# Kernel optimization log

Measured on AMD Instinct MI355X. Metric: run time of the kernel, lower is better.

The kernel has to match this reference:

```python
import jax, jax.numpy as jnp
import numpy as np

DELTA = 0.1  # fixed Gaussian temperature from __init__


def setup_inputs() -> dict:
    key = jax.random.key(0)
    k1, k2 = jax.random.split(key)
    B, T_TEXT, C = 16, 1024, 512
    T_FEAT = 4096  # static upper bound on sum(durations) per row (durations < 5 -> max 4*1024)
    x = jax.random.normal(k1, (B, T_TEXT, C), dtype=jnp.float32)
    durations = jax.random.randint(k2, (B, T_TEXT), 0, 5, dtype=jnp.int32)
    text_mask = jnp.ones((B, T_TEXT), dtype=bool)  # seqs_layout: valid text positions
    return {"x": x, "durations": durations, "text_mask": text_mask, "t_feat": T_FEAT}


def reference(x, durations, text_mask, t_feat):
    # x: (B, T_text, C); durations: (B, T_text) int; text_mask: (B, T_text) bool
    dtype = x.dtype
    d = durations.astype(dtype)
    out_lens = d.sum(axis=1)                                   # (B,)
    t = jnp.arange(t_feat, dtype=dtype)[None, :]               # (1, T_feat)
    y_mask = t < out_lens[:, None]                             # (B, T_feat) valid frames
    t = t * y_mask.astype(dtype)                               # zero out padded frames
    c = jnp.cumsum(d, axis=-1) - d * 0.5                       # (B, T_text) token centers
    # Gaussian energy over (frame, token) pairs: (B, T_feat, T_text)
    energy = -DELTA * (t[:, :, None] - c[:, None, :]) ** 2
    energy = jnp.where(text_mask[:, None, :], energy, -jnp.inf)
    p_attn = jax.nn.softmax(energy, axis=2)                    # softmax over T_text
    y = jnp.einsum("bft,btc->bfc", p_attn, x)                  # (B, T_feat, C)
    return y, out_lens.astype(jnp.int32)
```

## Files before the change

kernel.cpp:

```cpp
#include <hip/hip_runtime.h>
#include <stdint.h>


#define T_TEXT 1024
#define NEGK -0.14426950408889634f
#define WIN 12
#define WIN2F 169.0f

__global__ __launch_bounds__(1024) void scan_kernel(const int* __restrict__ dur,
                                                    const float* __restrict__ x,
                                                    float* __restrict__ c,
                                                    int* __restrict__ lens,
                                                    float* __restrict__ out_lens_f,
                                                    unsigned short* __restrict__ ft,
                                                    float* __restrict__ t0row,
                                                    int F) {
    const int b = blockIdx.x, tid = threadIdx.x;
    const int lane = tid & 63, wid = tid >> 6;
    const int d = dur[b * T_TEXT + tid];
    unsigned short* ftb = ft + (size_t)b * F;
    ((uint2*)ftb)[tid] = make_uint2(0x04000400u, 0x04000400u);

    __shared__ int wsum[16];
    __shared__ float clds[T_TEXT];
    __shared__ int sjhi0;
    if (tid == 0) sjhi0 = T_TEXT;

    int v = d;
#pragma unroll
    for (int off = 1; off < 64; off <<= 1) {
        int n = __shfl_up(v, off);
        if (lane >= off) v += n;
    }
    if (lane == 63) wsum[wid] = v;
    __syncthreads();
    if (tid < 16) {
        int s = wsum[tid];
#pragma unroll
        for (int off = 1; off < 16; off <<= 1) {
            int n = __shfl_up(s, off);
            if (tid >= off) s += n;
        }
        wsum[tid] = s;
    }
    __syncthreads();
    const int cum = v + (wid ? wsum[wid - 1] : 0);
    const float cv = (float)cum - 0.5f * (float)d;
    c[b * T_TEXT + tid] = cv;
    clds[tid] = cv;
    if (cum > WIN + 2 && cum - d <= WIN + 2) sjhi0 = tid;
    if (tid == T_TEXT - 1) { lens[b] = cum; out_lens_f[b] = (float)cum; }
    const int start = cum - d;
    for (int k = 0; k < d; ++k) ftb[start + k] = (unsigned short)tid;
    __syncthreads();

    const int jhi0 = sjhi0;
    if (tid < 512) {
        const float* xb = x + (size_t)b * T_TEXT * 512 + tid;
        float acc = 0.f, den = 0.f;
        for (int j = 0; j < jhi0; ++j) {
            const float cj = clds[j];
            const float w = exp2f(NEGK * cj * cj);
            acc += w * xb[(size_t)j * 512];
            den += w;
        }
        t0row[b * 512 + tid] = acc / den;
    }
}

__global__ __launch_bounds__(256, 4) void gauss_kernel(const float* __restrict__ x,
                                                       const float* __restrict__ c,
                                                       const int* __restrict__ lens,
                                                       const unsigned short* __restrict__ ft,
                                                       const float* __restrict__ t0row,
                                                       float* __restrict__ y,
                                                       int F) {
    const int C = 512;
    int bid = blockIdx.x;
    const int nwg = gridDim.x;
    if ((nwg & 7) == 0) bid = (bid & 7) * (nwg >> 3) + (bid >> 3);
    const int b = bid >> 8;
    const int f0 = (bid & 255) << 4;
    const int tid = threadIdx.x;
    const int fg = tid >> 7;
    const int chb = (tid & 127) << 2;

    const float* cb = c + b * T_TEXT;
    const unsigned short* ftb = ft + (size_t)b * F;
    const float* xb = x + (size_t)b * T_TEXT * C + chb;
    float* yb = y + ((size_t)b * F + f0) * C + chb;

    const int out_len = lens[b];
    int nvalid = out_len - f0;
    nvalid = nvalid < 0 ? 0 : (nvalid > 16 ? 16 : nvalid);

    if (nvalid < 16) {
        const float4 r = *(const float4*)&t0row[b * C + chb];
        for (int row = nvalid + fg; row < 16; row += 2)
            *(float4*)&yb[(size_t)row * C] = r;
    }

    if (nvalid > 0) {
        __shared__ float wlds[16][64];
        float4 acc[8];
        float den[8];
#pragma unroll
        for (int i = 0; i < 8; ++i) { acc[i] = make_float4(0.f, 0.f, 0.f, 0.f); den[i] = 0.f; }

        const int u = f0 - WIN - 2;
        int jlo = (u <= 0) ? 0 : (int)ftb[u < F ? u : F - 1];
        const int v = f0 + nvalid - 1 + WIN + 2;
        const int jhi = (v >= F) ? T_TEXT : (int)ftb[v];
        jlo &= ~3;

        for (int j0 = jlo; j0 < jhi; j0 += 64) {
            __syncthreads();
            {
                const int f = tid >> 4;
                const int tq = (tid & 15) << 2;
                const int j = j0 + tq;
                const float tf = (f < nvalid) ? (float)(f0 + f) : -3000.0f;
                float4 w4 = make_float4(0.f, 0.f, 0.f, 0.f);
                if (j < T_TEXT) {
                    const float4 c4 = *(const float4*)&cb[j];
                    const float d0 = tf - c4.x, d1 = tf - c4.y, d2 = tf - c4.z, d3 = tf - c4.w;
                    const float s0 = d0 * d0, s1 = d1 * d1, s2 = d2 * d2, s3 = d3 * d3;
                    if (j + 0 < jhi && s0 <= WIN2F) w4.x = exp2f(NEGK * s0);
                    if (j + 1 < jhi && s1 <= WIN2F) w4.y = exp2f(NEGK * s1);
                    if (j + 2 < jhi && s2 <= WIN2F) w4.z = exp2f(NEGK * s2);
                    if (j + 3 < jhi && s3 <= WIN2F) w4.w = exp2f(NEGK * s3);
                }
                *(float4*)&wlds[f][tq] = w4;
            }
            __syncthreads();

            int ntok = jhi - j0;
            if (ntok > 64) ntok = 64;
            for (int g = 0; g < ntok; g += 4) {
                float4 xv[4];
#pragma unroll
                for (int q = 0; q < 4; ++q) {
                    int jj = j0 + g + q;
                    jj = jj < T_TEXT ? jj : T_TEXT - 1;
                    xv[q] = *(const float4*)&xb[(size_t)jj * C];
                }
#pragma unroll
                for (int f = 0; f < 8; ++f) {
                    const float4 w4 = *(const float4*)&wlds[fg * 8 + f][g];
                    const float ws = (w4.x + w4.y) + (w4.z + w4.w);
                    if (ws != 0.f) {
                        acc[f].x += w4.x * xv[0].x; acc[f].y += w4.x * xv[0].y;
                        acc[f].z += w4.x * xv[0].z; acc[f].w += w4.x * xv[0].w;
                        acc[f].x += w4.y * xv[1].x; acc[f].y += w4.y * xv[1].y;
                        acc[f].z += w4.y * xv[1].z; acc[f].w += w4.y * xv[1].w;
                        acc[f].x += w4.z * xv[2].x; acc[f].y += w4.z * xv[2].y;
                        acc[f].z += w4.z * xv[2].z; acc[f].w += w4.z * xv[2].w;
                        acc[f].x += w4.w * xv[3].x; acc[f].y += w4.w * xv[3].y;
                        acc[f].z += w4.w * xv[3].z; acc[f].w += w4.w * xv[3].w;
                        den[f] += ws;
                    }
                }
            }
        }
#pragma unroll
        for (int f = 0; f < 8; ++f) {
            const int row = fg * 8 + f;
            if (row < nvalid) {
                const float inv = 1.0f / den[f];
                *(float4*)&yb[(size_t)row * C] =
                    make_float4(acc[f].x * inv, acc[f].y * inv, acc[f].z * inv, acc[f].w * inv);
            }
        }
    }
}

extern "C" void kernel_launch(void* const* d_in, const int* in_sizes, int n_in,
                              void* d_out, int out_size, void* d_ws, size_t ws_size,
                              hipStream_t stream) {
    const float* x = (const float*)d_in[0];
    const int* dur = (const int*)d_in[1];

    const int B = in_sizes[1] / T_TEXT;
    const int C = in_sizes[0] / in_sizes[1];
    const int F = (out_size / B - 1) / C;

    float* cbuf = (float*)d_ws;
    int* lens = (int*)((char*)d_ws + (size_t)B * T_TEXT * 4);
    unsigned short* ft = (unsigned short*)((char*)d_ws + 131072);
    float* t0row = (float*)((char*)d_ws + 262144);
    float* yout = (float*)d_out;
    float* out_lens_f = yout + (size_t)B * F * C;

    scan_kernel<<<B, T_TEXT, 0, stream>>>(dur, x, cbuf, lens, out_lens_f, ft, t0row, F);
    gauss_kernel<<<B * (F / 16), 256, 0, stream>>>(x, cbuf, lens, ft, t0row, yout, F);
}
```

Measured before the change: 39.28 us.

## Fuse duration scan into gauss kernel and locate token windows by binary search

Removes the separate scan kernel. Each gauss block now recomputes the prefix sum of durations for its batch row into shared memory, and finds the token window with binary searches over token centers instead of a frame-to-token lookup table. Padded rows compute the t=0 row locally instead of reading a precomputed one. Output stores become nontemporal. This saves one launch and the dependency between the two kernels, at the cost of redundant scan work in every block plus extra shared memory and barriers.

```diff
diff --git a/kernel.cpp b/kernel.cpp
--- a/kernel.cpp
+++ b/kernel.cpp
@@ -4,114 +4,103 @@
 
 #define T_TEXT 1024
 #define NEGK -0.14426950408889634f
-#define WIN 12
+#define CUT 13.5f
 #define WIN2F 169.0f
 
-__global__ __launch_bounds__(1024) void scan_kernel(const int* __restrict__ dur,
-                                                    const float* __restrict__ x,
-                                                    float* __restrict__ c,
-                                                    int* __restrict__ lens,
-                                                    float* __restrict__ out_lens_f,
-                                                    unsigned short* __restrict__ ft,
-                                                    float* __restrict__ t0row,
-                                                    int F) {
-    const int b = blockIdx.x, tid = threadIdx.x;
-    const int lane = tid & 63, wid = tid >> 6;
-    const int d = dur[b * T_TEXT + tid];
-    unsigned short* ftb = ft + (size_t)b * F;
-    ((uint2*)ftb)[tid] = make_uint2(0x04000400u, 0x04000400u);
+typedef float vfloat4 __attribute__((ext_vector_type(4)));
 
-    __shared__ int wsum[16];
-    __shared__ float clds[T_TEXT];
-    __shared__ int sjhi0;
-    if (tid == 0) sjhi0 = T_TEXT;
-
-    int v = d;
-#pragma unroll
-    for (int off = 1; off < 64; off <<= 1) {
-        int n = __shfl_up(v, off);
-        if (lane >= off) v += n;
-    }
-    if (lane == 63) wsum[wid] = v;
-    __syncthreads();
-    if (tid < 16) {
-        int s = wsum[tid];
-#pragma unroll
-        for (int off = 1; off < 16; off <<= 1) {
-            int n = __shfl_up(s, off);
-            if (tid >= off) s += n;
-        }
-        wsum[tid] = s;
-    }
-    __syncthreads();
-    const int cum = v + (wid ? wsum[wid - 1] : 0);
-    const float cv = (float)cum - 0.5f * (float)d;
-    c[b * T_TEXT + tid] = cv;
-    clds[tid] = cv;
-    if (cum > WIN + 2 && cum - d <= WIN + 2) sjhi0 = tid;
-    if (tid == T_TEXT - 1) { lens[b] = cum; out_lens_f[b] = (float)cum; }
-    const int start = cum - d;
-    for (int k = 0; k < d; ++k) ftb[start + k] = (unsigned short)tid;
-    __syncthreads();
-
-    const int jhi0 = sjhi0;
-    if (tid < 512) {
-        const float* xb = x + (size_t)b * T_TEXT * 512 + tid;
-        float acc = 0.f, den = 0.f;
-        for (int j = 0; j < jhi0; ++j) {
-            const float cj = clds[j];
-            const float w = exp2f(NEGK * cj * cj);
-            acc += w * xb[(size_t)j * 512];
-            den += w;
-        }
-        t0row[b * 512 + tid] = acc / den;
-    }
+__device__ __forceinline__ void nt_store4(float* p, float4 v) {
+    vfloat4 nv;
+    nv.x = v.x; nv.y = v.y; nv.z = v.z; nv.w = v.w;
+    __builtin_nontemporal_store(nv, (vfloat4*)p);
 }
 
 __global__ __launch_bounds__(256, 4) void gauss_kernel(const float* __restrict__ x,
-                                                       const float* __restrict__ c,
-                                                       const int* __restrict__ lens,
-                                                       const unsigned short* __restrict__ ft,
-                                                       const float* __restrict__ t0row,
+                                                       const int* __restrict__ dur,
                                                        float* __restrict__ y,
+                                                       float* __restrict__ out_lens_f,
                                                        int F) {
     const int C = 512;
     int bid = blockIdx.x;
     const int nwg = gridDim.x;
     if ((nwg & 7) == 0) bid = (bid & 7) * (nwg >> 3) + (bid >> 3);
-    const int b = bid >> 8;
-    const int f0 = (bid & 255) << 4;
+    const int nt = F >> 4;
+    const int b = bid / nt;
+    const int f0 = (bid - b * nt) << 4;
     const int tid = threadIdx.x;
+    const int lane = tid & 63, wid = tid >> 6;
     const int fg = tid >> 7;
     const int chb = (tid & 127) << 2;
 
-    const float* cb = c + b * T_TEXT;
-    const unsigned short* ftb = ft + (size_t)b * F;
+    __shared__ float clds[T_TEXT];
+    __shared__ float wlds[16][64];
+    __shared__ int wtot[4];
+
+    const int4 d4 = ((const int4*)(dur + b * T_TEXT))[tid];
+    const int p0 = d4.x, p1 = p0 + d4.y, p2 = p1 + d4.z, p3 = p2 + d4.w;
+    int s = p3;
+#pragma unroll
+    for (int off = 1; off < 64; off <<= 1) {
+        int n = __shfl_up(s, off);
+        if (lane >= off) s += n;
+    }
+    if (lane == 63) wtot[wid] = s;
+    __syncthreads();
+    int base = s - p3;
+    const int w0 = wtot[0], w1 = wtot[1], w2 = wtot[2], w3 = wtot[3];
+    const int out_len = ((w0 + w1) + (w2 + w3));
+    if (wid > 0) base += w0;
+    if (wid > 1) base += w1;
+    if (wid > 2) base += w2;
+    float4 cv;
+    cv.x = (float)(base + p0) - 0.5f * (float)d4.x;
+    cv.y = (float)(base + p1) - 0.5f * (float)d4.y;
+    cv.z = (float)(base + p2) - 0.5f * (float)d4.z;
+    cv.w = (float)(base + p3) - 0.5f * (float)d4.w;
+    *(float4*)&clds[tid << 2] = cv;
+    __syncthreads();
+
+    if (f0 == 0 && tid == 0) out_lens_f[b] = (float)out_len;
+
+    int nvalid = out_len - f0;
+    nvalid = nvalid < 0 ? 0 : (nvalid > 16 ? 16 : nvalid);
+
     const float* xb = x + (size_t)b * T_TEXT * C + chb;
     float* yb = y + ((size_t)b * F + f0) * C + chb;
 
-    const int out_len = lens[b];
-    int nvalid = out_len - f0;
-    nvalid = nvalid < 0 ? 0 : (nvalid > 16 ? 16 : nvalid);
-
     if (nvalid < 16) {
-        const float4 r = *(const float4*)&t0row[b * C + chb];
+        int lo = 0, hi = T_TEXT;
+        while (lo < hi) { int m = (lo + hi) >> 1; if (clds[m] <= CUT) lo = m + 1; else hi = m; }
+        const int jhi0 = lo;
+        float4 a = make_float4(0.f, 0.f, 0.f, 0.f);
+        float dn = 0.f;
+        for (int j = 0; j < jhi0; ++j) {
+            const float cj = clds[j];
+            const float w = exp2f(NEGK * cj * cj);
+            const float4 xv = *(const float4*)&xb[(size_t)j * C];
+            a.x += w * xv.x; a.y += w * xv.y; a.z += w * xv.z; a.w += w * xv.w;
+            dn += w;
+        }
+        const float inv = 1.0f / dn;
+        const float4 r = make_float4(a.x * inv, a.y * inv, a.z * inv, a.w * inv);
         for (int row = nvalid + fg; row < 16; row += 2)
-            *(float4*)&yb[(size_t)row * C] = r;
+            nt_store4(&yb[(size_t)row * C], r);
     }
 
     if (nvalid > 0) {
-        __shared__ float wlds[16][64];
         float4 acc[8];
         float den[8];
 #pragma unroll
         for (int i = 0; i < 8; ++i) { acc[i] = make_float4(0.f, 0.f, 0.f, 0.f); den[i] = 0.f; }
 
-        const int u = f0 - WIN - 2;
-        int jlo = (u <= 0) ? 0 : (int)ftb[u < F ? u : F - 1];
-        const int v = f0 + nvalid - 1 + WIN + 2;
-        const int jhi = (v >= F) ? T_TEXT : (int)ftb[v];
-        jlo &= ~3;
+        const float wlo = (float)f0 - CUT;
+        const float whi = (float)(f0 + nvalid - 1) + CUT;
+        int lo = 0, hi = T_TEXT;
+        while (lo < hi) { int m = (lo + hi) >> 1; if (clds[m] < wlo) lo = m + 1; else hi = m; }
+        const int jlo = lo & ~3;
+        hi = T_TEXT;
+        while (lo < hi) { int m = (lo + hi) >> 1; if (clds[m] <= whi) lo = m + 1; else hi = m; }
+        const int jhi = lo;
 
         for (int j0 = jlo; j0 < jhi; j0 += 64) {
             __syncthreads();
@@ -122,9 +111,9 @@
                 const float tf = (f < nvalid) ? (float)(f0 + f) : -3000.0f;
                 float4 w4 = make_float4(0.f, 0.f, 0.f, 0.f);
                 if (j < T_TEXT) {
-                    const float4 c4 = *(const float4*)&cb[j];
-                    const float d0 = tf - c4.x, d1 = tf - c4.y, d2 = tf - c4.z, d3 = tf - c4.w;
-                    const float s0 = d0 * d0, s1 = d1 * d1, s2 = d2 * d2, s3 = d3 * d3;
+                    const float4 c4 = *(const float4*)&clds[j];
+                    const float e0 = tf - c4.x, e1 = tf - c4.y, e2 = tf - c4.z, e3 = tf - c4.w;
+                    const float s0 = e0 * e0, s1 = e1 * e1, s2 = e2 * e2, s3 = e3 * e3;
                     if (j + 0 < jhi && s0 <= WIN2F) w4.x = exp2f(NEGK * s0);
                     if (j + 1 < jhi && s1 <= WIN2F) w4.y = exp2f(NEGK * s1);
                     if (j + 2 < jhi && s2 <= WIN2F) w4.z = exp2f(NEGK * s2);
@@ -167,8 +156,8 @@
             const int row = fg * 8 + f;
             if (row < nvalid) {
                 const float inv = 1.0f / den[f];
-                *(float4*)&yb[(size_t)row * C] =
-                    make_float4(acc[f].x * inv, acc[f].y * inv, acc[f].z * inv, acc[f].w * inv);
+                nt_store4(&yb[(size_t)row * C],
+                          make_float4(acc[f].x * inv, acc[f].y * inv, acc[f].z * inv, acc[f].w * inv));
             }
         }
     }
@@ -184,13 +173,8 @@
     const int C = in_sizes[0] / in_sizes[1];
     const int F = (out_size / B - 1) / C;
 
-    float* cbuf = (float*)d_ws;
-    int* lens = (int*)((char*)d_ws + (size_t)B * T_TEXT * 4);
-    unsigned short* ft = (unsigned short*)((char*)d_ws + 131072);
-    float* t0row = (float*)((char*)d_ws + 262144);
     float* yout = (float*)d_out;
     float* out_lens_f = yout + (size_t)B * F * C;
 
-    scan_kernel<<<B, T_TEXT, 0, stream>>>(dur, x, cbuf, lens, out_lens_f, ft, t0row, F);
-    gauss_kernel<<<B * (F / 16), 256, 0, stream>>>(x, cbuf, lens, ft, t0row, yout, F);
+    gauss_kernel<<<B * (F / 16), 256, 0, stream>>>(x, dur, yout, out_lens_f, F);
 }
```

Result: faster. 37.63 us (-4.2%).
